# Performance work log

Hardware: AMD Instinct MI355X
Metric: run time of the kernel (lower is better)

## Reference

```python
import jax, jax.numpy as jnp
import numpy as np

B, C, H, W = 4, 256, 64, 64
G, K, P = 4, 7, 3          # groups, kernel size, padding
RED = 32                   # out_channels // reduce_ratio
BN_EPS = 1e-5


def setup_inputs() -> dict:
    key = jax.random.key(0)
    ks = jax.random.split(key, 3)
    x = jax.random.normal(ks[0], (B, C, H, W), dtype=jnp.float32)
    w_reduce = jax.random.normal(ks[1], (RED, C), dtype=jnp.float32) * (1.0 / np.sqrt(C))
    bn_gamma = jnp.ones((RED,), dtype=jnp.float32)
    bn_beta = jnp.zeros((RED,), dtype=jnp.float32)
    w_span = jax.random.normal(ks[2], (K * K * G, RED), dtype=jnp.float32) * (1.0 / np.sqrt(RED))
    b_span = jnp.zeros((K * K * G,), dtype=jnp.float32)
    return {"x": x, "w_reduce": w_reduce, "bn_gamma": bn_gamma,
            "bn_beta": bn_beta, "w_span": w_span, "b_span": b_span}


def _involution(x, w_reduce, bn_gamma, bn_beta, w_span, b_span):
    # ---- dynamic kernel generation (stride=1 so AvgPool is identity) ----
    red = jnp.einsum('oc,bchw->bohw', w_reduce, x)                 # [B,RED,H,W]
    # BatchNorm2d forward with batch statistics (training-mode math)
    mean = red.mean(axis=(0, 2, 3), keepdims=True)
    var = red.var(axis=(0, 2, 3), keepdims=True)
    red_n = (red - mean) * jax.lax.rsqrt(var + BN_EPS)
    act = jax.nn.relu(red_n * bn_gamma[None, :, None, None] + bn_beta[None, :, None, None])
    ker = jnp.einsum('oc,bchw->bohw', w_span, act) + b_span[None, :, None, None]
    ker = ker.reshape(B, G, K * K, H, W)                           # [B,G,KK,H,W]

    # ---- unfold: K*K shifted views of the padded input ----
    xp = jnp.pad(x, ((0, 0), (0, 0), (P, P), (P, P)))
    patches = jnp.stack([xp[:, :, i:i + H, j:j + W]
                         for i in range(K) for j in range(K)], axis=2)  # [B,C,KK,H,W]
    patches = patches.reshape(B, G, C // G, K * K, H, W)

    # ---- per-pixel weighted neighborhood sum ----
    out = jnp.einsum('bgkhw,bgckhw->bgchw', ker, patches)
    return out.reshape(B, C, H, W)


def reference(x, w_reduce, bn_gamma, bn_beta, w_span, b_span):
    return _involution(x, w_reduce, bn_gamma, bn_beta, w_span, b_span)
```

## Files before the change

kernel.cpp:

```cpp
#include <hip/hip_runtime.h>

#define B_ 4
#define C_ 256
#define H_ 64
#define W_ 64
#define HW_ 4096
#define G_ 4
#define K_ 7
#define P_ 3
#define KK_ 49
#define KKG_ 196
#define RED_ 32
#define NPIX_ 16384
#define NSTAT_ 16384.0f
#define BN_EPS_ 1e-5f
#define OCH_ 28

#define CPB_ 8
#define TH_ 8
#define TRS_ 14
#define TRW_ 76

__global__ __launch_bounds__(256) void k_reduce(const float* __restrict__ x,
                                               const float* __restrict__ wr,
                                               float4* __restrict__ part,
                                               float* __restrict__ gstats) {
    const int tid = threadIdx.x;
    const int og  = blockIdx.y;
    const int bz  = blockIdx.z;
    if (blockIdx.x == 0 && og == 0 && bz == 0 && tid < 64) gstats[tid] = 0.0f;

    const int p2 = blockIdx.x * 256 + tid;
    const int b  = p2 >> 11;
    const int hw = (p2 & 2047) << 1;
    const float* xp = x + ((size_t)(b * C_ + bz * 64)) * HW_ + hw;
    const float* wp = wr + (og * 8) * C_ + bz * 64;

    float a[8][2];
#pragma unroll
    for (int oi = 0; oi < 8; ++oi) { a[oi][0] = 0.f; a[oi][1] = 0.f; }

#pragma unroll 8
    for (int cc = 0; cc < 64; ++cc) {
        const float2 v = *(const float2*)(xp + (size_t)cc * HW_);
#pragma unroll
        for (int oi = 0; oi < 8; ++oi) {
            const float wv = wp[oi * C_ + cc];
            a[oi][0] = fmaf(wv, v.x, a[oi][0]);
            a[oi][1] = fmaf(wv, v.y, a[oi][1]);
        }
    }

    const int slot = bz * 4 + og;
    float4* pp0 = part + (((size_t)(slot * 2 + 0)) << 14) + (p2 << 1);
    float4* pp1 = part + (((size_t)(slot * 2 + 1)) << 14) + (p2 << 1);
    pp0[0] = make_float4(a[0][0], a[1][0], a[2][0], a[3][0]);
    pp0[1] = make_float4(a[0][1], a[1][1], a[2][1], a[3][1]);
    pp1[0] = make_float4(a[4][0], a[5][0], a[6][0], a[7][0]);
    pp1[1] = make_float4(a[4][1], a[5][1], a[6][1], a[7][1]);
}

__global__ __launch_bounds__(256) void k_comb(const float4* __restrict__ part,
                                              float4* __restrict__ red,
                                              float* __restrict__ gsum,
                                              float* __restrict__ gsq) {
    __shared__ float lsum[4][8];
    const int tid  = threadIdx.x;
    const int lane = tid & 63;
    const int wv   = tid >> 6;
    const int oq   = blockIdx.y;
    const int og   = oq >> 1;
    const int half = oq & 1;
    const int p    = blockIdx.x * 256 + tid;

    float4 s = make_float4(0.f, 0.f, 0.f, 0.f);
#pragma unroll
    for (int bz = 0; bz < 4; ++bz) {
        const float4 v = part[(((size_t)((bz * 4 + og) * 2 + half)) << 14) + p];
        s.x += v.x; s.y += v.y; s.z += v.z; s.w += v.w;
    }
    red[((size_t)oq << 14) + p] = s;

    float s0 = s.x, s1 = s.y, s2 = s.z, s3 = s.w;
    float q0 = s.x*s.x, q1 = s.y*s.y, q2 = s.z*s.z, q3 = s.w*s.w;
#pragma unroll
    for (int off = 32; off > 0; off >>= 1) {
        s0 += __shfl_down(s0, off);  q0 += __shfl_down(q0, off);
        s1 += __shfl_down(s1, off);  q1 += __shfl_down(q1, off);
        s2 += __shfl_down(s2, off);  q2 += __shfl_down(q2, off);
        s3 += __shfl_down(s3, off);  q3 += __shfl_down(q3, off);
    }
    if (lane == 0) {
        lsum[wv][0] = s0; lsum[wv][1] = s1; lsum[wv][2] = s2; lsum[wv][3] = s3;
        lsum[wv][4] = q0; lsum[wv][5] = q1; lsum[wv][6] = q2; lsum[wv][7] = q3;
    }
    __syncthreads();
    if (tid < 8) {
        const float v = lsum[0][tid] + lsum[1][tid] + lsum[2][tid] + lsum[3][tid];
        float* dst = (tid < 4) ? &gsum[oq * 4 + tid] : &gsq[oq * 4 + (tid - 4)];
        atomicAdd(dst, v);
    }
}

__global__ __launch_bounds__(256) void k_span(const float4* __restrict__ red,
                                              const float* __restrict__ wspan,
                                              const float* __restrict__ bspan,
                                              const float* __restrict__ gsum,
                                              const float* __restrict__ gsq,
                                              const float* __restrict__ gamma,
                                              const float* __restrict__ beta,
                                              float* __restrict__ ker) {
    __shared__ float sc_l[RED_], sh_l[RED_];
    const int tid   = threadIdx.x;
    const int chunk = blockIdx.y;
    const int obase = chunk * OCH_;
    if (tid < RED_) {
        const float m   = gsum[tid] * (1.0f / NSTAT_);
        const float var = gsq[tid] * (1.0f / NSTAT_) - m * m;
        const float inv = rsqrtf(var + BN_EPS_);
        const float sc  = gamma[tid] * inv;
        sc_l[tid] = sc;
        sh_l[tid] = beta[tid] - m * sc;
    }
    __syncthreads();

    const int p  = blockIdx.x * 256 + tid;
    const int b  = p >> 12;
    const int hw = p & 4095;

    float act[RED_];
#pragma unroll
    for (int og = 0; og < 8; ++og) {
        const float4 v = red[((size_t)og << 14) + p];
        act[4*og+0] = v.x; act[4*og+1] = v.y; act[4*og+2] = v.z; act[4*og+3] = v.w;
    }
#pragma unroll
    for (int o = 0; o < RED_; ++o)
        act[o] = fmaxf(fmaf(act[o], sc_l[o], sh_l[o]), 0.0f);

    float* kp = ker + ((size_t)b * KKG_ + obase) * HW_ + hw;
    const float* wp = wspan + (size_t)obase * RED_;
#pragma unroll 4
    for (int o = 0; o < OCH_; ++o) {
        float s = bspan[obase + o];
#pragma unroll
        for (int c = 0; c < RED_; ++c)
            s = fmaf(wp[o * RED_ + c], act[c], s);
        kp[(size_t)o * HW_] = s;
    }
}

__global__ __launch_bounds__(256) void k_inv(const float* __restrict__ x,
                                             const float* __restrict__ ker,
                                             float* __restrict__ out) {
    __shared__ float tile[CPB_][TRS_][TRW_];
    const int tid = threadIdx.x;
    const int wg  = tid & 7;
    const int hq  = (tid >> 3) & 7;
    const int cq  = tid >> 6;
    const int bx  = blockIdx.x;
    const int ht  = bx & 7;
    const int cblk = (bx >> 3) & 31;
    const int b   = bx >> 8;
    const int h0  = ht << 3;
    const int c0  = cblk << 3;
    const int g   = c0 >> 6;
    const int w0  = wg << 3;
    const int h   = h0 + hq;

    const float4 fz = make_float4(0.f, 0.f, 0.f, 0.f);
#pragma unroll
    for (int it = 0; it < 7; ++it) {
        const int i   = it * 256 + tid;
        const int ci  = i / (TRS_ * 16);
        const int rem = i - ci * (TRS_ * 16);
        const int r   = rem >> 4;
        const int seg = rem & 15;
        const int hh  = h0 + r - P_;
        float4 v = fz;
        if (hh >= 0 && hh < H_)
            v = *(const float4*)(x + (((size_t)(b * C_ + c0 + ci)) << 12) + (hh << 6) + (seg << 2));
        *(float4*)&tile[ci][r][4 + (seg << 2)] = v;
    }
    if (tid < CPB_ * TRS_ * 2) {
        const int ci  = tid / (TRS_ * 2);
        const int rem = tid - ci * (TRS_ * 2);
        const int r   = rem >> 1;
        *(float4*)&tile[ci][r][(rem & 1) ? 68 : 0] = fz;
    }
    __syncthreads();

    const int cA = cq << 1;
    const float* kp = ker + (((size_t)b * KKG_ + g * KK_) << 12) + (h << 6) + w0;

    float accA[8], accB[8];
#pragma unroll
    for (int dw = 0; dw < 8; ++dw) { accA[dw] = 0.f; accB[dw] = 0.f; }

#pragma unroll
    for (int i = 0; i < K_; ++i) {
        const int r = hq + i;
        float wa[16], wb[16];
        const float* ta = &tile[cA][r][w0];
        const float* tb = &tile[cA + 1][r][w0];
#pragma unroll
        for (int t = 0; t < 4; ++t) {
            const float4 va = *(const float4*)(ta + (t << 2));
            const float4 vb = *(const float4*)(tb + (t << 2));
            wa[4*t+0]=va.x; wa[4*t+1]=va.y; wa[4*t+2]=va.z; wa[4*t+3]=va.w;
            wb[4*t+0]=vb.x; wb[4*t+1]=vb.y; wb[4*t+2]=vb.z; wb[4*t+3]=vb.w;
        }
#pragma unroll
        for (int j = 0; j < K_; ++j) {
            const float* kpp = kp + ((size_t)(i * K_ + j) << 12);
            const float4 k0 = *(const float4*)kpp;
            const float4 k1 = *(const float4*)(kpp + 4);
            const float kv[8] = {k0.x, k0.y, k0.z, k0.w, k1.x, k1.y, k1.z, k1.w};
#pragma unroll
            for (int dw = 0; dw < 8; ++dw) {
                accA[dw] = fmaf(kv[dw], wa[dw + j + 1], accA[dw]);
                accB[dw] = fmaf(kv[dw], wb[dw + j + 1], accB[dw]);
            }
        }
    }

    float* oA = out + (((size_t)(b * C_ + c0 + cA)) << 12) + (h << 6) + w0;
    *(float4*)(oA)     = make_float4(accA[0], accA[1], accA[2], accA[3]);
    *(float4*)(oA + 4) = make_float4(accA[4], accA[5], accA[6], accA[7]);
    float* oB = oA + HW_;
    *(float4*)(oB)     = make_float4(accB[0], accB[1], accB[2], accB[3]);
    *(float4*)(oB + 4) = make_float4(accB[4], accB[5], accB[6], accB[7]);
}

extern "C" void kernel_launch(void* const* d_in, const int* in_sizes, int n_in,
                              void* d_out, int out_size, void* d_ws, size_t ws_size,
                              hipStream_t stream) {
    const float* x     = (const float*)d_in[0];
    const float* wr    = (const float*)d_in[1];
    const float* gamma = (const float*)d_in[2];
    const float* beta  = (const float*)d_in[3];
    const float* wspan = (const float*)d_in[4];
    const float* bspan = (const float*)d_in[5];
    float* out = (float*)d_out;
    float* ws  = (float*)d_ws;

    float* red   = ws;
    float* gsum  = ws + 524288;
    float* gsq   = gsum + 32;
    float* ker   = ws + 524416;
    float* part  = ker;

    hipLaunchKernelGGL(k_reduce, dim3(32, 4, 4),  dim3(256), 0, stream, x, wr, (float4*)part, gsum);
    hipLaunchKernelGGL(k_comb,   dim3(64, 8),     dim3(256), 0, stream, (const float4*)part, (float4*)red, gsum, gsq);
    hipLaunchKernelGGL(k_span,   dim3(64, 7),     dim3(256), 0, stream, (const float4*)red, wspan, bspan, gsum, gsq, gamma, beta, ker);
    hipLaunchKernelGGL(k_inv,    dim3(1024),      dim3(256), 0, stream, x, ker, out);
}
```

Before: 64.28 us.

## Fuse four kernel launches into one cooperative kernel with grid syncs

Replaces the four separate launches (reduce, combine, span, involution) with one cooperative kernel of 512 blocks that separates the phases with grid-wide syncs. Each involution block now handles two tiles, and the shared tile width shrinks. The partial-sum buffer moves to its own workspace region so it no longer aliases ker. The aim is to remove inter-kernel launch gaps and tail effects, at the cost of grid-sync overhead, a capped 512-block grid, and lower occupancy in the involution phase.

```diff
diff --git a/kernel.cpp b/kernel.cpp
--- a/kernel.cpp
+++ b/kernel.cpp
@@ -1,25 +1,243 @@
 #include <hip/hip_runtime.h>
+#include <hip/hip_cooperative_groups.h>
+
+namespace cg = cooperative_groups;
 
 #define B_ 4
 #define C_ 256
 #define H_ 64
 #define W_ 64
 #define HW_ 4096
-#define G_ 4
 #define K_ 7
 #define P_ 3
 #define KK_ 49
 #define KKG_ 196
 #define RED_ 32
-#define NPIX_ 16384
 #define NSTAT_ 16384.0f
 #define BN_EPS_ 1e-5f
 #define OCH_ 28
 
 #define CPB_ 8
-#define TH_ 8
 #define TRS_ 14
-#define TRW_ 76
+#define TRW_ 72
+
+__global__ __launch_bounds__(256, 2) void k_fused(
+    const float* __restrict__ x, const float* __restrict__ wr,
+    const float* __restrict__ gamma, const float* __restrict__ beta,
+    const float* __restrict__ wspan, const float* __restrict__ bspan,
+    float4* __restrict__ part, float4* __restrict__ red,
+    float* __restrict__ gsum, float* __restrict__ gsq,
+    float* __restrict__ ker, float* __restrict__ out)
+{
+    __shared__ float smem[CPB_ * TRS_ * TRW_];
+    cg::grid_group grid = cg::this_grid();
+    const int id  = blockIdx.x;
+    const int tid = threadIdx.x;
+
+    {
+        const int bx = id & 31;
+        const int og = (id >> 5) & 3;
+        const int bz = id >> 7;
+        if (id == 0 && tid < 64) gsum[tid] = 0.0f;
+
+        const int p2 = bx * 256 + tid;
+        const int b  = p2 >> 11;
+        const int hw = (p2 & 2047) << 1;
+        const float* xp = x + ((size_t)(b * C_ + bz * 64)) * HW_ + hw;
+        const float* wp = wr + (og * 8) * C_ + bz * 64;
+
+        float a[8][2];
+#pragma unroll
+        for (int oi = 0; oi < 8; ++oi) { a[oi][0] = 0.f; a[oi][1] = 0.f; }
+
+#pragma unroll 8
+        for (int cc = 0; cc < 64; ++cc) {
+            const float2 v = *(const float2*)(xp + (size_t)cc * HW_);
+#pragma unroll
+            for (int oi = 0; oi < 8; ++oi) {
+                const float wv = wp[oi * C_ + cc];
+                a[oi][0] = fmaf(wv, v.x, a[oi][0]);
+                a[oi][1] = fmaf(wv, v.y, a[oi][1]);
+            }
+        }
+
+        const int slot = bz * 4 + og;
+        float4* pp0 = part + (((size_t)(slot * 2 + 0)) << 14) + (p2 << 1);
+        float4* pp1 = part + (((size_t)(slot * 2 + 1)) << 14) + (p2 << 1);
+        pp0[0] = make_float4(a[0][0], a[1][0], a[2][0], a[3][0]);
+        pp0[1] = make_float4(a[0][1], a[1][1], a[2][1], a[3][1]);
+        pp1[0] = make_float4(a[4][0], a[5][0], a[6][0], a[7][0]);
+        pp1[1] = make_float4(a[4][1], a[5][1], a[6][1], a[7][1]);
+    }
+    grid.sync();
+
+    {
+        float (*lsum)[8] = (float (*)[8])smem;
+        const int bx   = id & 63;
+        const int oq   = id >> 6;
+        const int og   = oq >> 1;
+        const int half = oq & 1;
+        const int lane = tid & 63;
+        const int wv   = tid >> 6;
+        const int p    = bx * 256 + tid;
+
+        float4 s = make_float4(0.f, 0.f, 0.f, 0.f);
+#pragma unroll
+        for (int bz = 0; bz < 4; ++bz) {
+            const float4 v = part[(((size_t)((bz * 4 + og) * 2 + half)) << 14) + p];
+            s.x += v.x; s.y += v.y; s.z += v.z; s.w += v.w;
+        }
+        red[((size_t)oq << 14) + p] = s;
+
+        float s0 = s.x, s1 = s.y, s2 = s.z, s3 = s.w;
+        float q0 = s.x*s.x, q1 = s.y*s.y, q2 = s.z*s.z, q3 = s.w*s.w;
+#pragma unroll
+        for (int off = 32; off > 0; off >>= 1) {
+            s0 += __shfl_down(s0, off);  q0 += __shfl_down(q0, off);
+            s1 += __shfl_down(s1, off);  q1 += __shfl_down(q1, off);
+            s2 += __shfl_down(s2, off);  q2 += __shfl_down(q2, off);
+            s3 += __shfl_down(s3, off);  q3 += __shfl_down(q3, off);
+        }
+        if (lane == 0) {
+            lsum[wv][0] = s0; lsum[wv][1] = s1; lsum[wv][2] = s2; lsum[wv][3] = s3;
+            lsum[wv][4] = q0; lsum[wv][5] = q1; lsum[wv][6] = q2; lsum[wv][7] = q3;
+        }
+        __syncthreads();
+        if (tid < 8) {
+            const float v = lsum[0][tid] + lsum[1][tid] + lsum[2][tid] + lsum[3][tid];
+            float* dst = (tid < 4) ? &gsum[oq * 4 + tid] : &gsq[oq * 4 + (tid - 4)];
+            atomicAdd(dst, v);
+        }
+    }
+    grid.sync();
+
+    if (id < 448) {
+        float* sc_l = smem;
+        float* sh_l = smem + 32;
+        const int bx    = id & 63;
+        const int chunk = id >> 6;
+        const int obase = chunk * OCH_;
+        if (tid < RED_) {
+            const float m   = gsum[tid] * (1.0f / NSTAT_);
+            const float var = gsq[tid] * (1.0f / NSTAT_) - m * m;
+            const float inv = rsqrtf(var + BN_EPS_);
+            const float sc  = gamma[tid] * inv;
+            sc_l[tid] = sc;
+            sh_l[tid] = beta[tid] - m * sc;
+        }
+        __syncthreads();
+
+        const int p  = bx * 256 + tid;
+        const int b  = p >> 12;
+        const int hw = p & 4095;
+
+        float act[RED_];
+#pragma unroll
+        for (int og = 0; og < 8; ++og) {
+            const float4 v = red[((size_t)og << 14) + p];
+            act[4*og+0] = v.x; act[4*og+1] = v.y; act[4*og+2] = v.z; act[4*og+3] = v.w;
+        }
+#pragma unroll
+        for (int o = 0; o < RED_; ++o)
+            act[o] = fmaxf(fmaf(act[o], sc_l[o], sh_l[o]), 0.0f);
+
+        float* kp = ker + ((size_t)b * KKG_ + obase) * HW_ + hw;
+        const float* wp = wspan + (size_t)obase * RED_;
+#pragma unroll 4
+        for (int o = 0; o < OCH_; ++o) {
+            float s = bspan[obase + o];
+#pragma unroll
+            for (int c = 0; c < RED_; ++c)
+                s = fmaf(wp[o * RED_ + c], act[c], s);
+            kp[(size_t)o * HW_] = s;
+        }
+    }
+    grid.sync();
+
+    {
+        float (*tile)[TRS_][TRW_] = (float (*)[TRS_][TRW_])smem;
+        const int wg  = tid & 7;
+        const int hq  = (tid >> 3) & 7;
+        const int cq  = tid >> 6;
+        const int w0  = wg << 3;
+        const float4 fz = make_float4(0.f, 0.f, 0.f, 0.f);
+
+#pragma unroll
+        for (int rep = 0; rep < 2; ++rep) {
+            const int tile_id = (id << 1) + rep;
+            const int ht   = tile_id & 7;
+            const int cblk = (tile_id >> 3) & 31;
+            const int b    = tile_id >> 8;
+            const int h0   = ht << 3;
+            const int c0   = cblk << 3;
+            const int g    = c0 >> 6;
+            const int h    = h0 + hq;
+
+            if (rep) __syncthreads();
+#pragma unroll
+            for (int it = 0; it < 7; ++it) {
+                const int i   = it * 256 + tid;
+                const int ci  = i / (TRS_ * 16);
+                const int rem = i - ci * (TRS_ * 16);
+                const int r   = rem >> 4;
+                const int seg = rem & 15;
+                const int hh  = h0 + r - P_;
+                float4 v = fz;
+                if (hh >= 0 && hh < H_)
+                    v = *(const float4*)(x + (((size_t)(b * C_ + c0 + ci)) << 12) + (hh << 6) + (seg << 2));
+                *(float4*)&tile[ci][r][4 + (seg << 2)] = v;
+            }
+            if (tid < CPB_ * TRS_ * 2) {
+                const int ci  = tid / (TRS_ * 2);
+                const int rem = tid - ci * (TRS_ * 2);
+                const int r   = rem >> 1;
+                *(float4*)&tile[ci][r][(rem & 1) ? 68 : 0] = fz;
+            }
+            __syncthreads();
+
+            const int cA = cq << 1;
+            const float* kp = ker + (((size_t)b * KKG_ + g * KK_) << 12) + (h << 6) + w0;
+
+            float accA[8], accB[8];
+#pragma unroll
+            for (int dw = 0; dw < 8; ++dw) { accA[dw] = 0.f; accB[dw] = 0.f; }
+
+#pragma unroll
+            for (int i = 0; i < K_; ++i) {
+                const int r = hq + i;
+                float wa[16], wb[16];
+                const float* ta = &tile[cA][r][w0];
+                const float* tb = &tile[cA + 1][r][w0];
+#pragma unroll
+                for (int t = 0; t < 4; ++t) {
+                    const float4 va = *(const float4*)(ta + (t << 2));
+                    const float4 vb = *(const float4*)(tb + (t << 2));
+                    wa[4*t+0]=va.x; wa[4*t+1]=va.y; wa[4*t+2]=va.z; wa[4*t+3]=va.w;
+                    wb[4*t+0]=vb.x; wb[4*t+1]=vb.y; wb[4*t+2]=vb.z; wb[4*t+3]=vb.w;
+                }
+#pragma unroll
+                for (int j = 0; j < K_; ++j) {
+                    const float* kpp = kp + ((size_t)(i * K_ + j) << 12);
+                    const float4 k0 = *(const float4*)kpp;
+                    const float4 k1 = *(const float4*)(kpp + 4);
+                    const float kv[8] = {k0.x, k0.y, k0.z, k0.w, k1.x, k1.y, k1.z, k1.w};
+#pragma unroll
+                    for (int dw = 0; dw < 8; ++dw) {
+                        accA[dw] = fmaf(kv[dw], wa[dw + j + 1], accA[dw]);
+                        accB[dw] = fmaf(kv[dw], wb[dw + j + 1], accB[dw]);
+                    }
+                }
+            }
+
+            float* oA = out + (((size_t)(b * C_ + c0 + cA)) << 12) + (h << 6) + w0;
+            *(float4*)(oA)     = make_float4(accA[0], accA[1], accA[2], accA[3]);
+            *(float4*)(oA + 4) = make_float4(accA[4], accA[5], accA[6], accA[7]);
+            float* oB = oA + HW_;
+            *(float4*)(oB)     = make_float4(accB[0], accB[1], accB[2], accB[3]);
+            *(float4*)(oB + 4) = make_float4(accB[4], accB[5], accB[6], accB[7]);
+        }
+    }
+}
 
 __global__ __launch_bounds__(256) void k_reduce(const float* __restrict__ x,
                                                const float* __restrict__ wr,
@@ -39,7 +257,6 @@
     float a[8][2];
 #pragma unroll
     for (int oi = 0; oi < 8; ++oi) { a[oi][0] = 0.f; a[oi][1] = 0.f; }
-
 #pragma unroll 8
     for (int cc = 0; cc < 64; ++cc) {
         const float2 v = *(const float2*)(xp + (size_t)cc * HW_);
@@ -50,7 +267,6 @@
             a[oi][1] = fmaf(wv, v.y, a[oi][1]);
         }
     }
-
     const int slot = bz * 4 + og;
     float4* pp0 = part + (((size_t)(slot * 2 + 0)) << 14) + (p2 << 1);
     float4* pp1 = part + (((size_t)(slot * 2 + 1)) << 14) + (p2 << 1);
@@ -244,14 +460,25 @@
     float* out = (float*)d_out;
     float* ws  = (float*)d_ws;
 
-    float* red   = ws;
-    float* gsum  = ws + 524288;
-    float* gsq   = gsum + 32;
-    float* ker   = ws + 524416;
-    float* part  = ker;
-
-    hipLaunchKernelGGL(k_reduce, dim3(32, 4, 4),  dim3(256), 0, stream, x, wr, (float4*)part, gsum);
-    hipLaunchKernelGGL(k_comb,   dim3(64, 8),     dim3(256), 0, stream, (const float4*)part, (float4*)red, gsum, gsq);
-    hipLaunchKernelGGL(k_span,   dim3(64, 7),     dim3(256), 0, stream, (const float4*)red, wspan, bspan, gsum, gsq, gamma, beta, ker);
-    hipLaunchKernelGGL(k_inv,    dim3(1024),      dim3(256), 0, stream, x, ker, out);
-}
+    float*  redf  = ws;
+    float*  gsum  = ws + 524288;
+    float*  gsq   = gsum + 32;
+    float*  ker   = ws + 524416;
+    float*  partf = ws + 524416 + 3211264;
+    float4* red   = (float4*)redf;
+    float4* part  = (float4*)partf;
+
+    void* kargs[] = {
+        (void*)&x, (void*)&wr, (void*)&gamma, (void*)&beta,
+        (void*)&wspan, (void*)&bspan, (void*)&part, (void*)&red,
+        (void*)&gsum, (void*)&gsq, (void*)&ker, (void*)&out
+    };
+    hipError_t err = hipLaunchCooperativeKernel((void*)k_fused, dim3(512), dim3(256),
+                                                kargs, 0, stream);
+    if (err != hipSuccess) {
+        hipLaunchKernelGGL(k_reduce, dim3(32, 4, 4), dim3(256), 0, stream, x, wr, part, gsum);
+        hipLaunchKernelGGL(k_comb,   dim3(64, 8),    dim3(256), 0, stream, part, red, gsum, gsq);
+        hipLaunchKernelGGL(k_span,   dim3(64, 7),    dim3(256), 0, stream, red, wspan, bspan, gsum, gsq, gamma, beta, ker);
+        hipLaunchKernelGGL(k_inv,    dim3(1024),     dim3(256), 0, stream, x, ker, out);
+    }
+}
```

Result: slower. 247.2 us (+284.6%).
